# Performance work log

Measured on AMD Instinct MI355X. Metric: run time of the kernel, lower is better.

The kernel has to match this reference:

```python
import jax, jax.numpy as jnp
import numpy as np

N = 50000
NEG_SLOPE = 0.2


def gat_conv(x, src, dst, W, a_src, a_dst, b):
    # PyG GATConv, heads=1: h = xW; e_ij = LeakyReLU(a_src.h_j + a_dst.h_i);
    # softmax over edges sharing destination i; out_i = sum_j alpha_ij h_j + b.
    h = x @ W                                   # [N, F]
    as_ = h @ a_src                             # [N]
    ad_ = h @ a_dst                             # [N]
    e = jax.nn.leaky_relu(as_[src] + ad_[dst], NEG_SLOPE)  # [E]
    m = jax.ops.segment_max(e, dst, num_segments=N)        # per-dst max
    m = jnp.where(jnp.isfinite(m), m, 0.0)
    p = jnp.exp(e - m[dst])
    denom = jax.ops.segment_sum(p, dst, num_segments=N)
    alpha = p / jnp.maximum(denom[dst], 1e-16)             # [E]
    out = jax.ops.segment_sum(alpha[:, None] * h[src], dst, num_segments=N)
    return out + b


def setup_inputs() -> dict:
    key = jax.random.key(0)
    ks = jax.random.split(key, 12)
    E, L = 800000, 262144
    F_in, F_mid, F_out = 128, 64, 32
    x = jax.random.normal(ks[0], (N, F_in), dtype=jnp.float32)
    edge_index = jax.random.randint(ks[1], (2, E), 0, N, dtype=jnp.int32)
    edge_label_index = jax.random.randint(ks[2], (2, L), 0, N, dtype=jnp.int32)
    s1 = 1.0 / np.sqrt(F_in)
    s2 = 1.0 / np.sqrt(F_mid)
    return {
        "x": x,
        "edge_index": edge_index,
        "edge_label_index": edge_label_index,
        "W1": jax.random.normal(ks[3], (F_in, F_mid), jnp.float32) * s1,
        "a_src1": jax.random.normal(ks[4], (F_mid,), jnp.float32) * s2,
        "a_dst1": jax.random.normal(ks[5], (F_mid,), jnp.float32) * s2,
        "b1": jnp.zeros((F_mid,), jnp.float32),
        "W2": jax.random.normal(ks[6], (F_mid, F_out), jnp.float32) * s2,
        "a_src2": jax.random.normal(ks[7], (F_out,), jnp.float32) * (1.0 / np.sqrt(F_out)),
        "a_dst2": jax.random.normal(ks[8], (F_out,), jnp.float32) * (1.0 / np.sqrt(F_out)),
        "b2": jnp.zeros((F_out,), jnp.float32),
    }


def reference(x, edge_index, edge_label_index, W1, a_src1, a_dst1, b1, W2, a_src2, a_dst2, b2):
    # add self-loops (PyG GATConv default add_self_loops=True)
    loops = jnp.arange(N, dtype=edge_index.dtype)
    src = jnp.concatenate([edge_index[0], loops])
    dst = jnp.concatenate([edge_index[1], loops])
    z = jax.nn.relu(gat_conv(x, src, dst, W1, a_src1, a_dst1, b1))
    z = gat_conv(z, src, dst, W2, a_src2, a_dst2, b2)
    # dot-product decode over candidate edges
    return jnp.sum(z[edge_label_index[0]] * z[edge_label_index[1]], axis=-1)
```

## Files before the change

kernel.cpp:

```cpp
#include <hip/hip_runtime.h>

#define NN 50000
#define NEG 0.2f
#define NBUCK 196
#define NBLK 208
#define SLOT 64

__device__ __forceinline__ float leaky(float v) { return v > 0.0f ? v : NEG * v; }

__device__ __forceinline__ unsigned f2bf(float x) {
    unsigned u = __float_as_uint(x);
    return (u + 0x7FFFu + ((u >> 16) & 1u)) >> 16;
}
__device__ __forceinline__ float bflo(unsigned g) { return __uint_as_float(g << 16); }
__device__ __forceinline__ float bfhi(unsigned g) { return __uint_as_float(g & 0xFFFF0000u); }

__global__ __launch_bounds__(256) void k_part_gemm1(
        const int* __restrict__ ei, int E, int CHUNK,
        int* __restrict__ bh, unsigned int* __restrict__ part,
        const float* __restrict__ x, const float* __restrict__ W,
        const float* __restrict__ a_src, const float* __restrict__ a_dst,
        unsigned int* __restrict__ hu, float* __restrict__ as_, float* __restrict__ ad_) {
    __shared__ float xs[4][8][128];
    __shared__ int hist[NBUCK];
    int tid = threadIdx.x;
    if (blockIdx.x < NBLK) {
        int b = blockIdx.x;
        if (tid < NBUCK) hist[tid] = 0;
        __syncthreads();
        int beg = b * CHUNK;
        int end = min(beg + CHUNK, E);
        for (int i = beg + tid; i < end; i += 256) {
            int sv = ei[i], dv = ei[E + i];
            int k = dv >> 8;
            int slot = atomicAdd(&hist[k], 1);
            if (slot < SLOT)
                part[(k * NBLK + b) * SLOT + slot] =
                    (unsigned)sv | ((unsigned)(dv & 255) << 16);
        }
        __syncthreads();
        if (tid < NBUCK) bh[b * NBUCK + tid] = min(hist[tid], SLOT);
        return;
    }
    int gblock = blockIdx.x - NBLK;
    int wl = tid >> 6;
    int lane = tid & 63;
    int base = (gblock * 4 + wl) * 8;
    if (base >= NN) return;
#pragma unroll
    for (int n = 0; n < 8; ++n) {
        int node = base + n;
        xs[wl][n][lane]      = x[node * 128 + lane];
        xs[wl][n][lane + 64] = x[node * 128 + 64 + lane];
    }
    float acc[8] = {0, 0, 0, 0, 0, 0, 0, 0};
#pragma unroll 8
    for (int kg = 0; kg < 32; ++kg) {
        float w0 = W[(4 * kg + 0) * 64 + lane];
        float w1 = W[(4 * kg + 1) * 64 + lane];
        float w2 = W[(4 * kg + 2) * 64 + lane];
        float w3 = W[(4 * kg + 3) * 64 + lane];
#pragma unroll
        for (int n = 0; n < 8; ++n) {
            float4 xv = *(const float4*)&xs[wl][n][kg * 4];
            acc[n] = fmaf(xv.x, w0, fmaf(xv.y, w1, fmaf(xv.z, w2, fmaf(xv.w, w3, acc[n]))));
        }
    }
    float pa = a_src[lane], pd = a_dst[lane];
#pragma unroll
    for (int n = 0; n < 8; ++n) {
        int node = base + n;
        unsigned my = f2bf(acc[n]);
        unsigned nb = __shfl_down(my, 1, 64);
        if ((lane & 1) == 0) hu[node * 32 + (lane >> 1)] = my | (nb << 16);
        float s = acc[n] * pa;
        float d = acc[n] * pd;
#pragma unroll
        for (int off = 32; off > 0; off >>= 1) {
            s += __shfl_xor(s, off, 64);
            d += __shfl_xor(d, off, 64);
        }
        if (lane == 0) { as_[node] = s; ad_[node] = d; }
    }
}

__global__ __launch_bounds__(256) void k_csr(
        const unsigned int* __restrict__ part, const int* __restrict__ bh,
        int2* __restrict__ rc, unsigned short* __restrict__ csr_src) {
    int k = blockIdx.x;
    int tid = threadIdx.x;
    int dst = (k << 8) + tid;
    __shared__ int lhist[256], roff[256], wsum[4];
    lhist[tid] = (dst < NN) ? 1 : 0;
    __syncthreads();
    int rl = 0;
    const unsigned int* myslot = part;
    if (tid < NBLK) {
        rl = bh[tid * NBUCK + k];
        myslot = part + (k * NBLK + tid) * SLOT;
        for (int i = 0; i < rl; ++i) atomicAdd(&lhist[myslot[i] >> 16], 1);
    }
    __syncthreads();
    int lane = tid & 63, w = tid >> 6;
    int v = lhist[tid];
    int inc = v;
#pragma unroll
    for (int off = 1; off < 64; off <<= 1) {
        int t = __shfl_up(inc, off, 64);
        if (lane >= off) inc += t;
    }
    if (lane == 63) wsum[w] = inc;
    __syncthreads();
    int wpre = 0;
    for (int q = 0; q < w; ++q) wpre += wsum[q];
    int excl = wpre + inc - v;
    int cbase = k * NBLK * SLOT;
    roff[tid] = cbase + excl;
    if (dst < NN) rc[dst] = make_int2(cbase + excl, v);
    __syncthreads();
    if (dst < NN) {
        int pos = atomicAdd(&roff[tid], 1);
        csr_src[pos] = (unsigned short)dst;
    }
    if (tid < NBLK) {
        for (int i = 0; i < rl; ++i) {
            unsigned e = myslot[i];
            int pos = atomicAdd(&roff[e >> 16], 1);
            csr_src[pos] = (unsigned short)(e & 0xFFFFu);
        }
    }
}

__global__ __launch_bounds__(256) void k_aggr1g2(
        const int2* __restrict__ rc, const unsigned short* __restrict__ csr_src,
        const float* __restrict__ as_, const float* __restrict__ ad_,
        const unsigned int* __restrict__ hu, const float* __restrict__ b1,
        const float* __restrict__ W2, const float* __restrict__ a2s,
        const float* __restrict__ a2d,
        unsigned int* __restrict__ hu2, float* __restrict__ as2,
        float* __restrict__ ad2) {
    __shared__ float w2s[64 * 32];
    int tid = threadIdx.x;
    int f = tid & 15;
    int dst = blockIdx.x * 16 + (tid >> 4);
    int2 rcv = rc[dst];
    float ad = ad_[dst];
#pragma unroll
    for (int i = 0; i < 8; ++i) w2s[tid + 256 * i] = W2[tid + 256 * i];
    __syncthreads();
    int start = rcv.x, deg = rcv.y;
    float a0 = 0, a1 = 0, a2 = 0, a3 = 0, ssum;

    if (deg <= 32) {
        int nA = min(deg, 16);
        int sA = 0, sB = 0;
        float eA = -1e30f, eB = -1e30f;
        if (f < nA) { sA = csr_src[start + f]; eA = leaky(as_[sA] + ad); }
        if (16 + f < deg) { sB = csr_src[start + 16 + f]; eB = leaky(as_[sB] + ad); }
        float m = fmaxf(eA, eB);
#pragma unroll
        for (int off = 8; off > 0; off >>= 1) m = fmaxf(m, __shfl_xor(m, off, 16));
        float pA = (f < nA) ? __expf(eA - m) : 0.0f;
        float pB = (16 + f < deg) ? __expf(eB - m) : 0.0f;
        ssum = pA + pB;
#pragma unroll
        for (int off = 8; off > 0; off >>= 1) ssum += __shfl_xor(ssum, off, 16);
        int t = 0;
        for (; t + 4 <= nA; t += 4) {
            int s0 = __shfl(sA, t, 16), s1 = __shfl(sA, t + 1, 16);
            int s2 = __shfl(sA, t + 2, 16), s3 = __shfl(sA, t + 3, 16);
            float p0 = __shfl(pA, t, 16), p1 = __shfl(pA, t + 1, 16);
            float p2 = __shfl(pA, t + 2, 16), p3 = __shfl(pA, t + 3, 16);
            uint2 g0 = *(const uint2*)&hu[s0 * 32 + 2 * f];
            uint2 g1 = *(const uint2*)&hu[s1 * 32 + 2 * f];
            uint2 g2 = *(const uint2*)&hu[s2 * 32 + 2 * f];
            uint2 g3 = *(const uint2*)&hu[s3 * 32 + 2 * f];
            a0 = fmaf(p0, bflo(g0.x), a0); a1 = fmaf(p0, bfhi(g0.x), a1);
            a2 = fmaf(p0, bflo(g0.y), a2); a3 = fmaf(p0, bfhi(g0.y), a3);
            a0 = fmaf(p1, bflo(g1.x), a0); a1 = fmaf(p1, bfhi(g1.x), a1);
            a2 = fmaf(p1, bflo(g1.y), a2); a3 = fmaf(p1, bfhi(g1.y), a3);
            a0 = fmaf(p2, bflo(g2.x), a0); a1 = fmaf(p2, bfhi(g2.x), a1);
            a2 = fmaf(p2, bflo(g2.y), a2); a3 = fmaf(p2, bfhi(g2.y), a3);
            a0 = fmaf(p3, bflo(g3.x), a0); a1 = fmaf(p3, bfhi(g3.x), a1);
            a2 = fmaf(p3, bflo(g3.y), a2); a3 = fmaf(p3, bfhi(g3.y), a3);
        }
        for (; t < nA; ++t) {
            int sv = __shfl(sA, t, 16);
            float pv = __shfl(pA, t, 16);
            uint2 g = *(const uint2*)&hu[sv * 32 + 2 * f];
            a0 = fmaf(pv, bflo(g.x), a0); a1 = fmaf(pv, bfhi(g.x), a1);
            a2 = fmaf(pv, bflo(g.y), a2); a3 = fmaf(pv, bfhi(g.y), a3);
        }
        for (t = 16; t < deg; ++t) {
            int sv = __shfl(sB, t - 16, 16);
            float pv = __shfl(pB, t - 16, 16);
            uint2 g = *(const uint2*)&hu[sv * 32 + 2 * f];
            a0 = fmaf(pv, bflo(g.x), a0); a1 = fmaf(pv, bfhi(g.x), a1);
            a2 = fmaf(pv, bflo(g.y), a2); a3 = fmaf(pv, bfhi(g.y), a3);
        }
    } else {
        float m = -1e30f;
        for (int base = 0; base < deg; base += 16) {
            int j = base + f;
            if (j < deg) m = fmaxf(m, leaky(as_[csr_src[start + j]] + ad));
        }
#pragma unroll
        for (int off = 8; off > 0; off >>= 1) m = fmaxf(m, __shfl_xor(m, off, 16));
        ssum = 0.0f;
        for (int base = 0; base < deg; base += 16) {
            int j = base + f;
            int sj = 0;
            float pj = 0.0f;
            if (j < deg) {
                sj = csr_src[start + j];
                pj = __expf(leaky(as_[sj] + ad) - m);
            }
            ssum += pj;
            int lim = min(16, deg - base);
            for (int t = 0; t < lim; ++t) {
                int sv = __shfl(sj, t, 16);
                float pv = __shfl(pj, t, 16);
                uint2 g = *(const uint2*)&hu[sv * 32 + 2 * f];
                a0 = fmaf(pv, bflo(g.x), a0); a1 = fmaf(pv, bfhi(g.x), a1);
                a2 = fmaf(pv, bflo(g.y), a2); a3 = fmaf(pv, bfhi(g.y), a3);
            }
        }
#pragma unroll
        for (int off = 8; off > 0; off >>= 1) ssum += __shfl_xor(ssum, off, 16);
    }

    float inv = 1.0f / ssum;
    float4 bb = *(const float4*)&b1[4 * f];
    float z0 = fmaxf(fmaf(a0, inv, bb.x), 0.0f);
    float z1 = fmaxf(fmaf(a1, inv, bb.y), 0.0f);
    float z2 = fmaxf(fmaf(a2, inv, bb.z), 0.0f);
    float z3 = fmaxf(fmaf(a3, inv, bb.w), 0.0f);

    float h0 = 0.0f, h1 = 0.0f;
#pragma unroll 4
    for (int t = 0; t < 16; ++t) {
        float y0 = __shfl(z0, t, 16);
        float y1 = __shfl(z1, t, 16);
        float y2 = __shfl(z2, t, 16);
        float y3 = __shfl(z3, t, 16);
        const float2* wp = (const float2*)&w2s[(4 * t) * 32 + 2 * f];
        float2 w0v = wp[0];
        float2 w1v = wp[16];
        float2 w2v = wp[32];
        float2 w3v = wp[48];
        h0 = fmaf(y0, w0v.x, fmaf(y1, w1v.x, fmaf(y2, w2v.x, fmaf(y3, w3v.x, h0))));
        h1 = fmaf(y0, w0v.y, fmaf(y1, w1v.y, fmaf(y2, w2v.y, fmaf(y3, w3v.y, h1))));
    }
    float2 av = *(const float2*)&a2s[2 * f];
    float2 dv = *(const float2*)&a2d[2 * f];
    float sa = fmaf(h0, av.x, h1 * av.y);
    float sd = fmaf(h0, dv.x, h1 * dv.y);
#pragma unroll
    for (int off = 8; off > 0; off >>= 1) {
        sa += __shfl_xor(sa, off, 16);
        sd += __shfl_xor(sd, off, 16);
    }
    if (f == 0) { as2[dst] = sa; ad2[dst] = sd; }
    hu2[dst * 16 + f] = f2bf(h0) | (f2bf(h1) << 16);
}

__global__ void k_aggr2(const int2* __restrict__ rc,
                        const unsigned short* __restrict__ csr_src,
                        const float* __restrict__ as_, const float* __restrict__ ad_,
                        const unsigned int* __restrict__ hu2, const float* __restrict__ b,
                        float* __restrict__ out) {
    int gid = blockIdx.x * blockDim.x + threadIdx.x;
    int dst = gid >> 4;
    int f = gid & 15;
    if (dst >= NN) return;
    int2 rcv = rc[dst];
    int start = rcv.x, deg = rcv.y;
    float ad = ad_[dst];
    float a0 = 0, a1 = 0, ssum;

    if (deg <= 32) {
        int nA = min(deg, 16);
        int sA = 0, sB = 0;
        float eA = -1e30f, eB = -1e30f;
        if (f < nA) { sA = csr_src[start + f]; eA = leaky(as_[sA] + ad); }
        if (16 + f < deg) { sB = csr_src[start + 16 + f]; eB = leaky(as_[sB] + ad); }
        float m = fmaxf(eA, eB);
#pragma unroll
        for (int off = 8; off > 0; off >>= 1) m = fmaxf(m, __shfl_xor(m, off, 16));
        float pA = (f < nA) ? __expf(eA - m) : 0.0f;
        float pB = (16 + f < deg) ? __expf(eB - m) : 0.0f;
        ssum = pA + pB;
#pragma unroll
        for (int off = 8; off > 0; off >>= 1) ssum += __shfl_xor(ssum, off, 16);
        int t = 0;
        for (; t + 4 <= nA; t += 4) {
            int s0 = __shfl(sA, t, 16), s1 = __shfl(sA, t + 1, 16);
            int s2 = __shfl(sA, t + 2, 16), s3 = __shfl(sA, t + 3, 16);
            float p0 = __shfl(pA, t, 16), p1 = __shfl(pA, t + 1, 16);
            float p2 = __shfl(pA, t + 2, 16), p3 = __shfl(pA, t + 3, 16);
            unsigned g0 = hu2[s0 * 16 + f];
            unsigned g1 = hu2[s1 * 16 + f];
            unsigned g2 = hu2[s2 * 16 + f];
            unsigned g3 = hu2[s3 * 16 + f];
            a0 = fmaf(p0, bflo(g0), a0); a1 = fmaf(p0, bfhi(g0), a1);
            a0 = fmaf(p1, bflo(g1), a0); a1 = fmaf(p1, bfhi(g1), a1);
            a0 = fmaf(p2, bflo(g2), a0); a1 = fmaf(p2, bfhi(g2), a1);
            a0 = fmaf(p3, bflo(g3), a0); a1 = fmaf(p3, bfhi(g3), a1);
        }
        for (; t < nA; ++t) {
            int sv = __shfl(sA, t, 16);
            float pv = __shfl(pA, t, 16);
            unsigned g = hu2[sv * 16 + f];
            a0 = fmaf(pv, bflo(g), a0); a1 = fmaf(pv, bfhi(g), a1);
        }
        for (t = 16; t < deg; ++t) {
            int sv = __shfl(sB, t - 16, 16);
            float pv = __shfl(pB, t - 16, 16);
            unsigned g = hu2[sv * 16 + f];
            a0 = fmaf(pv, bflo(g), a0); a1 = fmaf(pv, bfhi(g), a1);
        }
    } else {
        float m = -1e30f;
        for (int base = 0; base < deg; base += 16) {
            int j = base + f;
            if (j < deg) m = fmaxf(m, leaky(as_[csr_src[start + j]] + ad));
        }
#pragma unroll
        for (int off = 8; off > 0; off >>= 1) m = fmaxf(m, __shfl_xor(m, off, 16));
        ssum = 0.0f;
        for (int base = 0; base < deg; base += 16) {
            int j = base + f;
            int sj = 0;
            float pj = 0.0f;
            if (j < deg) {
                sj = csr_src[start + j];
                pj = __expf(leaky(as_[sj] + ad) - m);
            }
            ssum += pj;
            int lim = min(16, deg - base);
            for (int t = 0; t < lim; ++t) {
                int sv = __shfl(sj, t, 16);
                float pv = __shfl(pj, t, 16);
                unsigned g = hu2[sv * 16 + f];
                a0 = fmaf(pv, bflo(g), a0); a1 = fmaf(pv, bfhi(g), a1);
            }
        }
#pragma unroll
        for (int off = 8; off > 0; off >>= 1) ssum += __shfl_xor(ssum, off, 16);
    }

    float inv = 1.0f / ssum;
    float2 bb = *(const float2*)&b[2 * f];
    float2 r;
    r.x = fmaf(a0, inv, bb.x);
    r.y = fmaf(a1, inv, bb.y);
    *(float2*)&out[dst * 32 + 2 * f] = r;
}

__global__ void k_decode(const int* __restrict__ eli, int L,
                         const float* __restrict__ z2, float* __restrict__ out) {
    int gid = blockIdx.x * blockDim.x + threadIdx.x;
    int pair = gid >> 2;
    int f8 = gid & 3;
    if (pair >= L) return;
    int i = 0, j = 0;
    if (f8 == 0) { i = eli[pair]; j = eli[L + pair]; }
    i = __shfl(i, (threadIdx.x & 63) & ~3, 64);
    j = __shfl(j, (threadIdx.x & 63) & ~3, 64);
    const float4* zi = (const float4*)&z2[i * 32 + f8 * 8];
    const float4* zj = (const float4*)&z2[j * 32 + f8 * 8];
    float4 a0 = zi[0], a1 = zi[1];
    float4 b0 = zj[0], b1 = zj[1];
    float v = a0.x * b0.x + a0.y * b0.y + a0.z * b0.z + a0.w * b0.w
            + a1.x * b1.x + a1.y * b1.y + a1.z * b1.z + a1.w * b1.w;
#pragma unroll
    for (int off = 2; off > 0; off >>= 1) v += __shfl_xor(v, off, 4);
    if (f8 == 0) out[pair] = v;
}

extern "C" void kernel_launch(void* const* d_in, const int* in_sizes, int n_in,
                              void* d_out, int out_size, void* d_ws, size_t ws_size,
                              hipStream_t stream) {
    const float* x     = (const float*)d_in[0];
    const int*   ei    = (const int*)d_in[1];
    const int*   eli   = (const int*)d_in[2];
    const float* W1    = (const float*)d_in[3];
    const float* asrc1 = (const float*)d_in[4];
    const float* adst1 = (const float*)d_in[5];
    const float* b1    = (const float*)d_in[6];
    const float* W2    = (const float*)d_in[7];
    const float* asrc2 = (const float*)d_in[8];
    const float* adst2 = (const float*)d_in[9];
    const float* b2    = (const float*)d_in[10];
    float* out = (float*)d_out;

    const int E = in_sizes[1] / 2;
    const int L = in_sizes[2] / 2;
    const int CHUNK = (E + NBLK - 1) / NBLK;

    float* ws  = (float*)d_ws;
    unsigned int* hu  = (unsigned int*)ws;
    unsigned int* hu2 = hu + NN * 32;
    float* z2  = (float*)(hu2 + NN * 16);
    float* as1 = z2 + NN * 32;
    float* ad1 = as1 + NN;
    float* as2 = ad1 + NN;
    float* ad2 = as2 + NN;
    int2* rc  = (int2*)(ad2 + NN);
    int* bh   = (int*)(rc + NN);
    unsigned int*   part    = (unsigned int*)(bh + NBLK * NBUCK);
    unsigned short* csr_src = (unsigned short*)(part + NBUCK * NBLK * SLOT);

    const int GB = (NN / 8 + 3) / 4;

    k_part_gemm1<<<NBLK + GB, 256, 0, stream>>>(ei, E, CHUNK, bh, part,
                                                x, W1, asrc1, adst1, hu, as1, ad1);
    k_csr<<<NBUCK, 256, 0, stream>>>(part, bh, rc, csr_src);

    k_aggr1g2<<<NN / 16, 256, 0, stream>>>(rc, csr_src, as1, ad1, hu, b1,
                                           W2, asrc2, adst2, hu2, as2, ad2);

    k_aggr2<<<(NN * 16 + 255) / 256, 256, 0, stream>>>(
        rc, csr_src, as2, ad2, hu2, b2, z2);

    k_decode<<<(L * 4 + 255) / 256, 256, 0, stream>>>(eli, L, z2, out);
}
```

Measured before the change: 193.6 us.

## Compute first-layer GEMM with bf16 MFMA instead of scalar FMA

Replaces the scalar fp32 FMA loop for x@W1 with MFMA 16x16x32 bf16 instructions. Each wave handles 16 nodes and all 64 output columns, and the transposed bf16 copy of W is staged in shared memory. x is converted to bf16 on load. The attention dot products are reduced across 16 lanes with shuffles. This cuts ALU work and x staging through LDS, at the cost of lower GEMM input precision and of every block converting W into LDS.

```diff
diff --git a/kernel.cpp b/kernel.cpp
--- a/kernel.cpp
+++ b/kernel.cpp
@@ -5,6 +5,10 @@
 #define NBUCK 196
 #define NBLK 208
 #define SLOT 64
+#define WTS 136
+
+typedef __attribute__((ext_vector_type(8))) short bf16x8;
+typedef __attribute__((ext_vector_type(4))) float f32x4;
 
 __device__ __forceinline__ float leaky(float v) { return v > 0.0f ? v : NEG * v; }
 
@@ -21,7 +25,7 @@
         const float* __restrict__ x, const float* __restrict__ W,
         const float* __restrict__ a_src, const float* __restrict__ a_dst,
         unsigned int* __restrict__ hu, float* __restrict__ as_, float* __restrict__ ad_) {
-    __shared__ float xs[4][8][128];
+    __shared__ unsigned short wt[64 * WTS];
     __shared__ int hist[NBUCK];
     int tid = threadIdx.x;
     if (blockIdx.x < NBLK) {
@@ -42,45 +46,73 @@
         if (tid < NBUCK) bh[b * NBUCK + tid] = min(hist[tid], SLOT);
         return;
     }
-    int gblock = blockIdx.x - NBLK;
+    for (int i = tid; i < 128 * 64; i += 256) {
+        int k = i >> 6, n = i & 63;
+        wt[n * WTS + k] = (unsigned short)f2bf(W[i]);
+    }
+    __syncthreads();
     int wl = tid >> 6;
     int lane = tid & 63;
-    int base = (gblock * 4 + wl) * 8;
-    if (base >= NN) return;
-#pragma unroll
-    for (int n = 0; n < 8; ++n) {
-        int node = base + n;
-        xs[wl][n][lane]      = x[node * 128 + lane];
-        xs[wl][n][lane + 64] = x[node * 128 + 64 + lane];
-    }
-    float acc[8] = {0, 0, 0, 0, 0, 0, 0, 0};
-#pragma unroll 8
-    for (int kg = 0; kg < 32; ++kg) {
-        float w0 = W[(4 * kg + 0) * 64 + lane];
-        float w1 = W[(4 * kg + 1) * 64 + lane];
-        float w2 = W[(4 * kg + 2) * 64 + lane];
-        float w3 = W[(4 * kg + 3) * 64 + lane];
-#pragma unroll
-        for (int n = 0; n < 8; ++n) {
-            float4 xv = *(const float4*)&xs[wl][n][kg * 4];
-            acc[n] = fmaf(xv.x, w0, fmaf(xv.y, w1, fmaf(xv.z, w2, fmaf(xv.w, w3, acc[n]))));
-        }
-    }
-    float pa = a_src[lane], pd = a_dst[lane];
-#pragma unroll
-    for (int n = 0; n < 8; ++n) {
-        int node = base + n;
-        unsigned my = f2bf(acc[n]);
-        unsigned nb = __shfl_down(my, 1, 64);
-        if ((lane & 1) == 0) hu[node * 32 + (lane >> 1)] = my | (nb << 16);
-        float s = acc[n] * pa;
-        float d = acc[n] * pd;
-#pragma unroll
-        for (int off = 32; off > 0; off >>= 1) {
-            s += __shfl_xor(s, off, 64);
-            d += __shfl_xor(d, off, 64);
-        }
-        if (lane == 0) { as_[node] = s; ad_[node] = d; }
+    int c15 = lane & 15, quad = lane >> 4;
+    int mt = (blockIdx.x - NBLK) * 4 + wl;
+    if (mt >= NN / 16) return;
+
+    bf16x8 bf0[4], bf1[4], bf2[4], bf3[4];
+#pragma unroll
+    for (int ks = 0; ks < 4; ++ks) {
+        int ko = ks * 32 + quad * 8;
+        bf0[ks] = *(const bf16x8*)&wt[(c15)      * WTS + ko];
+        bf1[ks] = *(const bf16x8*)&wt[(16 + c15) * WTS + ko];
+        bf2[ks] = *(const bf16x8*)&wt[(32 + c15) * WTS + ko];
+        bf3[ks] = *(const bf16x8*)&wt[(48 + c15) * WTS + ko];
+    }
+    const float* xr = x + (mt * 16 + c15) * 128;
+    bf16x8 af[4];
+#pragma unroll
+    for (int ks = 0; ks < 4; ++ks) {
+        int ko = ks * 32 + quad * 8;
+        float4 u0 = *(const float4*)&xr[ko];
+        float4 u1 = *(const float4*)&xr[ko + 4];
+        bf16x8 a;
+        a[0] = (short)f2bf(u0.x); a[1] = (short)f2bf(u0.y);
+        a[2] = (short)f2bf(u0.z); a[3] = (short)f2bf(u0.w);
+        a[4] = (short)f2bf(u1.x); a[5] = (short)f2bf(u1.y);
+        a[6] = (short)f2bf(u1.z); a[7] = (short)f2bf(u1.w);
+        af[ks] = a;
+    }
+    f32x4 c0 = {0, 0, 0, 0}, c1 = {0, 0, 0, 0}, c2 = {0, 0, 0, 0}, c3 = {0, 0, 0, 0};
+#pragma unroll
+    for (int ks = 0; ks < 4; ++ks) {
+        c0 = __builtin_amdgcn_mfma_f32_16x16x32_bf16(af[ks], bf0[ks], c0, 0, 0, 0);
+        c1 = __builtin_amdgcn_mfma_f32_16x16x32_bf16(af[ks], bf1[ks], c1, 0, 0, 0);
+        c2 = __builtin_amdgcn_mfma_f32_16x16x32_bf16(af[ks], bf2[ks], c2, 0, 0, 0);
+        c3 = __builtin_amdgcn_mfma_f32_16x16x32_bf16(af[ks], bf3[ks], c3, 0, 0, 0);
+    }
+    float pa0 = a_src[c15], pa1 = a_src[16 + c15], pa2 = a_src[32 + c15], pa3 = a_src[48 + c15];
+    float pd0 = a_dst[c15], pd1 = a_dst[16 + c15], pd2 = a_dst[32 + c15], pd3 = a_dst[48 + c15];
+#pragma unroll
+    for (int r = 0; r < 4; ++r) {
+        int nd = mt * 16 + quad * 4 + r;
+        float s = c0[r] * pa0 + c1[r] * pa1 + c2[r] * pa2 + c3[r] * pa3;
+        float d = c0[r] * pd0 + c1[r] * pd1 + c2[r] * pd2 + c3[r] * pd3;
+#pragma unroll
+        for (int off = 8; off > 0; off >>= 1) {
+            s += __shfl_xor(s, off, 16);
+            d += __shfl_xor(d, off, 16);
+        }
+        if (c15 == 0) { as_[nd] = s; ad_[nd] = d; }
+        unsigned m0 = f2bf(c0[r]), m1 = f2bf(c1[r]), m2 = f2bf(c2[r]), m3 = f2bf(c3[r]);
+        unsigned n0 = __shfl_down(m0, 1, 64);
+        unsigned n1 = __shfl_down(m1, 1, 64);
+        unsigned n2 = __shfl_down(m2, 1, 64);
+        unsigned n3 = __shfl_down(m3, 1, 64);
+        if ((c15 & 1) == 0) {
+            int base = nd * 32 + (c15 >> 1);
+            hu[base]      = m0 | (n0 << 16);
+            hu[base + 8]  = m1 | (n1 << 16);
+            hu[base + 16] = m2 | (n2 << 16);
+            hu[base + 24] = m3 | (n3 << 16);
+        }
     }
 }
 
@@ -411,7 +443,7 @@
     unsigned int*   part    = (unsigned int*)(bh + NBLK * NBUCK);
     unsigned short* csr_src = (unsigned short*)(part + NBUCK * NBLK * SLOT);
 
-    const int GB = (NN / 8 + 3) / 4;
+    const int GB = (NN / 16 + 3) / 4;
 
     k_part_gemm1<<<NBLK + GB, 256, 0, stream>>>(ei, E, CHUNK, bh, part,
                                                 x, W1, asrc1, adst1, hu, as1, ad1);
```

Measured after the change: 181.1 us. 6.5% less time.
